# Performance work log

Measured on AMD Instinct MI355X. Metric: run time of the kernel, lower is better.

## Reference

```python
import jax, jax.numpy as jnp
import numpy as np

N_NODES = 10000
N_EDGES = 160000
D_IN = 128
D_EMB = 512
D_HID = 256
GAT_SLOPE = 0.2   # PyG GATv2Conv default negative_slope
MLP_SLOPE = 0.1   # relu_alpha


def _glorot(key, shape):
    fan_in, fan_out = shape[0], shape[-1]
    lim = np.sqrt(6.0 / (fan_in + fan_out))
    return jax.random.uniform(key, shape, jnp.float32, -lim, lim)


def setup_inputs() -> dict:
    key = jax.random.key(0)
    ks = jax.random.split(key, 20)
    inp = {
        'x': jax.random.normal(ks[0], (N_NODES, D_IN), jnp.float32),
        'edge_index': jax.random.randint(ks[1], (2, N_EDGES), 0, N_NODES, jnp.int64),
    }
    # GATv2 layers: (Wl, Wr, att, bias) each
    dims = [(D_IN, D_EMB), (D_EMB, D_EMB), (D_EMB, D_EMB)]
    for i, (di, do) in enumerate(dims, start=1):
        inp[f'Wl{i}'] = _glorot(ks[2 + 4 * i], (di, do))
        inp[f'Wr{i}'] = _glorot(ks[3 + 4 * i], (di, do))
        inp[f'att{i}'] = _glorot(ks[4 + 4 * i], (1, do))[0]
        inp[f'b{i}'] = jnp.zeros((do,), jnp.float32)
    # MLP
    inp['A1'] = _glorot(ks[2], (D_EMB, D_HID)); inp['c1'] = jnp.zeros((D_HID,), jnp.float32)
    inp['A2'] = _glorot(ks[3], (D_HID, D_HID)); inp['c2'] = jnp.zeros((D_HID,), jnp.float32)
    inp['A3'] = _glorot(ks[4], (D_HID, 1));     inp['c3'] = jnp.zeros((1,), jnp.float32)
    return inp


def gatv2_conv(x, src, dst, Wl, Wr, att, bias):
    # PyG GATv2Conv, heads=1: xl = source transform, xr = target transform
    xl = x @ Wl                                   # [N, D]
    xr = x @ Wr                                   # [N, D]
    # per-edge attention logit: att . leaky_relu(xl[src] + xr[dst])
    e = jax.nn.leaky_relu(xl[src] + xr[dst], GAT_SLOPE) @ att   # [E]
    # segment softmax over incoming edges of each dst node
    emax = jax.ops.segment_max(e, dst, num_segments=N_NODES)    # [N]
    w = jnp.exp(e - emax[dst])
    denom = jax.ops.segment_sum(w, dst, num_segments=N_NODES)   # [N]
    alpha = w / (denom[dst] + 1e-16)                             # [E]
    out = jax.ops.segment_sum(alpha[:, None] * xl[src], dst, num_segments=N_NODES)
    return out + bias


def reference(x, edge_index, Wl1, Wr1, att1, b1, Wl2, Wr2, att2, b2,
              Wl3, Wr3, att3, b3, A1, c1, A2, c2, A3, c3):
    src, dst = edge_index[0], edge_index[1]
    h = jnp.tanh(gatv2_conv(x, src, dst, Wl1, Wr1, att1, b1))
    h = jnp.tanh(gatv2_conv(h, src, dst, Wl2, Wr2, att2, b2))
    h = jnp.tanh(gatv2_conv(h, src, dst, Wl3, Wr3, att3, b3))
    h = jax.nn.leaky_relu(h @ A1 + c1, MLP_SLOPE)
    h = jax.nn.leaky_relu(h @ A2 + c2, MLP_SLOPE)
    logits = h @ A3 + c3                          # [N, 1]
    return jax.nn.softmax(logits, axis=0)         # softmax over nodes
```

## Files before the change

kernel.cpp:

```cpp
#include <hip/hip_runtime.h>
#include <hip/hip_bf16.h>

#define N_NODES 10000
#define N_EDGES 160000
#define D_IN    128
#define D_EMB   512
#define D_HID   256

typedef unsigned short u16;
typedef __attribute__((ext_vector_type(8))) short short8;
typedef __attribute__((ext_vector_type(4))) float floatx4;

__device__ __forceinline__ float bf2f(u16 u) {
    union { unsigned int i; float f; } v; v.i = ((unsigned int)u) << 16; return v.f;
}
__device__ __forceinline__ u16 f2bf(float f) {
    union { float f; unsigned int i; } v; v.f = f;
    unsigned int x = v.i;
    return (u16)((x + 0x7fffu + ((x >> 16) & 1u)) >> 16);
}
__device__ __forceinline__ float inval(const void* p, int fp32, int idx) {
    return fp32 ? ((const float*)p)[idx] : bf2f(((const u16*)p)[idx]);
}

__device__ __forceinline__ void gld_lds16(const u16* g, u16* l) {
    __builtin_amdgcn_global_load_lds((const __attribute__((address_space(1))) void*)g,
                                     (__attribute__((address_space(3))) void*)l,
                                     16, 0, 0);
}

__device__ __forceinline__ int edge_src(const int* __restrict__ ei, int flg, int e) {
    int v = flg ? ei[2 * e] : ei[e];
    return min(max(v, 0), N_NODES - 1);
}
__device__ __forceinline__ int edge_dst(const int* __restrict__ ei, int flg, int e) {
    int v = flg ? ei[2 * N_EDGES + 2 * e] : ei[N_EDGES + e];
    return min(max(v, 0), N_NODES - 1);
}

__global__ void sentinel_kernel(float* out, int n) {
    int i = blockIdx.x * 256 + threadIdx.x;
    if (i < n) out[i] = 1.0f;
}

__global__ __launch_bounds__(256)
void detect_zero_kernel(const int* __restrict__ ei, const u16* __restrict__ xu,
                        int* flag, int* counts, float* logits) {
    int gid = blockIdx.x * 256 + threadIdx.x;
    for (int i = gid; i < N_NODES; i += gridDim.x * 256) { counts[i] = 0; logits[i] = 0.f; }
    if (blockIdx.x != 0) return;
    __shared__ int s_or[256];
    __shared__ int s_cnt[256];
    int t = threadIdx.x;
    int v = 0;
    for (int k = t; k < 4096; k += 256) v |= ei[1 + 2 * k];
    int c = 0;
    for (int k = t; k < 4096; k += 256) {
        u16 u = xu[k];
        int ex = (u >> 7) & 0xFF;
        bool plaus = (u == 0) || (ex >= 64 && ex <= 191);
        if (!plaus) c++;
    }
    s_or[t] = v; s_cnt[t] = c;
    __syncthreads();
    for (int off = 128; off > 0; off >>= 1) {
        if (t < off) { s_or[t] |= s_or[t + off]; s_cnt[t] += s_cnt[t + off]; }
        __syncthreads();
    }
    if (t == 0) {
        flag[0] = (s_or[0] == 0) ? 1 : 0;
        flag[1] = (s_cnt[0] > 256) ? 1 : 0;
    }
}

struct ConvJobs {
    const void* src[10];
    u16* dh[10];
    u16* dl[10];
    int rows[10], cols[10], trans[10];
    int cum[11];
    int njobs;
};

__global__ __launch_bounds__(256)
void convert_fused_kernel(ConvJobs jobs, const int* __restrict__ flag) {
    int idx = blockIdx.x * 256 + threadIdx.x;
    if (idx >= jobs.cum[jobs.njobs]) return;
    int fp32 = flag[1];
    int jb = 0;
    while (idx >= jobs.cum[jb + 1]) jb++;
    int local = idx - jobs.cum[jb];
    float v = inval(jobs.src[jb], fp32, local);
    u16 hi = f2bf(v);
    int o;
    if (jobs.trans[jb]) {
        int r = local / jobs.cols[jb], c = local % jobs.cols[jb];
        o = c * jobs.rows[jb] + r;
    } else o = local;
    jobs.dh[jb][o] = hi;
    if (jobs.dl[jb]) jobs.dl[jb][o] = f2bf(v - bf2f(hi));
}

__global__ void count_edges_kernel(const int* __restrict__ ei, const int* __restrict__ flag,
                                   int* counts) {
    int e = blockIdx.x * 256 + threadIdx.x;
    if (e < N_EDGES) atomicAdd(&counts[edge_dst(ei, flag[0], e)], 1);
}

__global__ __launch_bounds__(256)
void scan_counts_kernel(int* counts, int* rowptr) {
    __shared__ int part[256];
    int tid = threadIdx.x;
    const int CH = 40;
    int base = tid * CH;
    int loc[CH];
    int s = 0;
    #pragma unroll
    for (int i = 0; i < CH; i++) {
        int idx = base + i;
        int c = (idx < N_NODES) ? counts[idx] : 0;
        loc[i] = s; s += c;
    }
    part[tid] = s;
    __syncthreads();
    for (int off = 1; off < 256; off <<= 1) {
        int v = part[tid];
        int add = (tid >= off) ? part[tid - off] : 0;
        __syncthreads();
        part[tid] = v + add;
        __syncthreads();
    }
    int pre = (tid > 0) ? part[tid - 1] : 0;
    #pragma unroll
    for (int i = 0; i < CH; i++) {
        int idx = base + i;
        if (idx < N_NODES) { int v = pre + loc[i]; rowptr[idx] = v; counts[idx] = v; }
    }
    if (tid == 255) rowptr[N_NODES] = part[255];
}

__global__ void fill_esrcp_kernel(const int* __restrict__ ei, const int* __restrict__ flag,
                                  int* counts, int* esrcp) {
    int e = blockIdx.x * 256 + threadIdx.x;
    if (e < N_EDGES) {
        int flg = flag[0];
        int pos = atomicAdd(&counts[edge_dst(ei, flg, e)], 1);
        if (pos >= 0 && pos < N_EDGES) esrcp[pos] = edge_src(ei, flg, e);
    }
}

__global__ __launch_bounds__(256)
void gemm_dual_kernel(const u16* __restrict__ Ah, const u16* __restrict__ Al,
                      const u16* __restrict__ B0h, const u16* __restrict__ B1h,
                      u16* __restrict__ C0, u16* __restrict__ C1,
                      int M, int N, int K)
{
    __shared__ u16 sAh[128 * 32];
    __shared__ u16 sAl[128 * 32];
    __shared__ u16 sBh[128 * 32];
    int nb = N >> 7;
    int half = (int)blockIdx.x >= nb;
    int bx = half ? (blockIdx.x - nb) : blockIdx.x;
    const u16* BTh = half ? B1h : B0h;
    u16* Cf = half ? C1 : C0;

    int tid = threadIdx.x;
    int lane = tid & 63, wv = tid >> 6;
    int l15 = lane & 15, l4 = lane >> 4;
    int wr = (wv >> 1) * 64, wc = (wv & 1) * 64;
    int m0 = blockIdx.y * 128, n0 = bx * 128;

    int i0 = tid, i1 = tid + 256;
    int r0 = i0 >> 2, b0 = i0 & 3, sb0 = b0 ^ ((r0 >> 1) & 3);
    int r1 = i1 >> 2, b1 = i1 & 3, sb1 = b1 ^ ((r1 >> 1) & 3);
    int gr0 = min(m0 + r0, M - 1), gr1 = min(m0 + r1, M - 1);
    const u16* a0p = Ah + (size_t)gr0 * K + sb0 * 8;
    const u16* a1p = Ah + (size_t)gr1 * K + sb1 * 8;
    const u16* l0p = Al + (size_t)gr0 * K + sb0 * 8;
    const u16* l1p = Al + (size_t)gr1 * K + sb1 * 8;
    const u16* bb0p = BTh + (size_t)(n0 + r0) * K + sb0 * 8;
    const u16* bb1p = BTh + (size_t)(n0 + r1) * K + sb1 * 8;
    u16* lA0 = &sAh[(size_t)(wv * 64) * 8];
    u16* lA1 = &sAh[(size_t)(256 + wv * 64) * 8];
    u16* lL0 = &sAl[(size_t)(wv * 64) * 8];
    u16* lL1 = &sAl[(size_t)(256 + wv * 64) * 8];
    u16* lB0 = &sBh[(size_t)(wv * 64) * 8];
    u16* lB1 = &sBh[(size_t)(256 + wv * 64) * 8];

    floatx4 acc[4][4];
    #pragma unroll
    for (int i = 0; i < 4; i++)
        #pragma unroll
        for (int j = 0; j < 4; j++) acc[i][j] = (floatx4){0.f, 0.f, 0.f, 0.f};

    int aoff[4], boff[4];
    #pragma unroll
    for (int i = 0; i < 4; i++) {
        int arow = wr + i * 16 + l15;
        aoff[i] = arow * 32 + ((l4 ^ ((arow >> 1) & 3)) << 3);
        int bcol = wc + i * 16 + l15;
        boff[i] = bcol * 32 + ((l4 ^ ((bcol >> 1) & 3)) << 3);
    }

    for (int kk = 0; kk < K; kk += 32) {
        __syncthreads();
        gld_lds16(a0p + kk, lA0);
        gld_lds16(a1p + kk, lA1);
        gld_lds16(l0p + kk, lL0);
        gld_lds16(l1p + kk, lL1);
        gld_lds16(bb0p + kk, lB0);
        gld_lds16(bb1p + kk, lB1);
        __syncthreads();

        short8 ah[4], al[4];
        #pragma unroll
        for (int i = 0; i < 4; i++) {
            ah[i] = *(const short8*)(&sAh[aoff[i]]);
            al[i] = *(const short8*)(&sAl[aoff[i]]);
        }
        #pragma unroll
        for (int j = 0; j < 4; j++) {
            short8 bh = *(const short8*)(&sBh[boff[j]]);
            #pragma unroll
            for (int i = 0; i < 4; i++) {
                acc[i][j] = __builtin_amdgcn_mfma_f32_16x16x32_bf16(ah[i], bh, acc[i][j], 0, 0, 0);
                acc[i][j] = __builtin_amdgcn_mfma_f32_16x16x32_bf16(al[i], bh, acc[i][j], 0, 0, 0);
            }
        }
    }

    #pragma unroll
    for (int j = 0; j < 4; j++) {
        int col = n0 + wc + j * 16 + l15;
        #pragma unroll
        for (int i = 0; i < 4; i++) {
            #pragma unroll
            for (int r = 0; r < 4; r++) {
                int row = m0 + wr + i * 16 + l4 * 4 + r;
                if (row < M) Cf[(size_t)row * N + col] = f2bf(acc[i][j][r]);
            }
        }
    }
}

template<int FUSE>
__global__ __launch_bounds__(256)
void gemm_mlp64_kernel(const u16* __restrict__ Ah, const u16* __restrict__ Al,
                       const u16* __restrict__ BTh,
                       u16* __restrict__ Ch, u16* __restrict__ Cl,
                       const void* __restrict__ biasraw,
                       const void* __restrict__ A3raw, float* __restrict__ logits,
                       const int* __restrict__ flag,
                       int M, int N, int K)
{
    __shared__ u16 sAh[64 * 32];
    __shared__ u16 sAl[64 * 32];
    __shared__ u16 sBh[64 * 32];
    int tid = threadIdx.x;
    int lane = tid & 63, wv = tid >> 6;
    int l15 = lane & 15, l4 = lane >> 4;
    int m0 = blockIdx.y * 64, n0 = blockIdx.x * 64;

    int r = (tid >> 2), blk = tid & 3, sb = blk ^ ((r >> 1) & 3);
    int gr = min(m0 + r, M - 1);
    const u16* ap = Ah + (size_t)gr * K + sb * 8;
    const u16* lp = Al + (size_t)gr * K + sb * 8;
    const u16* bp = BTh + (size_t)(n0 + r) * K + sb * 8;
    u16* lA = &sAh[(size_t)(wv * 64) * 8];
    u16* lL = &sAl[(size_t)(wv * 64) * 8];
    u16* lB = &sBh[(size_t)(wv * 64) * 8];

    floatx4 acc[4];
    #pragma unroll
    for (int j = 0; j < 4; j++) acc[j] = (floatx4){0.f, 0.f, 0.f, 0.f};

    int arow = wv * 16 + l15;
    int aoff = arow * 32 + ((l4 ^ ((arow >> 1) & 3)) << 3);
    int boff[4];
    #pragma unroll
    for (int j = 0; j < 4; j++) {
        int bcol = j * 16 + l15;
        boff[j] = bcol * 32 + ((l4 ^ ((bcol >> 1) & 3)) << 3);
    }

    for (int kk = 0; kk < K; kk += 32) {
        __syncthreads();
        gld_lds16(ap + kk, lA);
        gld_lds16(lp + kk, lL);
        gld_lds16(bp + kk, lB);
        __syncthreads();

        short8 ah = *(const short8*)(&sAh[aoff]);
        short8 al = *(const short8*)(&sAl[aoff]);
        #pragma unroll
        for (int j = 0; j < 4; j++) {
            short8 bh = *(const short8*)(&sBh[boff[j]]);
            acc[j] = __builtin_amdgcn_mfma_f32_16x16x32_bf16(ah, bh, acc[j], 0, 0, 0);
            acc[j] = __builtin_amdgcn_mfma_f32_16x16x32_bf16(al, bh, acc[j], 0, 0, 0);
        }
    }

    const int fp32 = flag[1];
    float lsum[4] = {0.f, 0.f, 0.f, 0.f};
    #pragma unroll
    for (int j = 0; j < 4; j++) {
        int col = n0 + j * 16 + l15;
        float bv = inval(biasraw, fp32, col);
        float a3 = FUSE ? inval(A3raw, fp32, col) : 0.f;
        #pragma unroll
        for (int rr = 0; rr < 4; rr++) {
            int row = m0 + wv * 16 + l4 * 4 + rr;
            if (row < M) {
                float v = acc[j][rr] + bv;
                v = v > 0.f ? v : 0.1f * v;
                if (FUSE) {
                    lsum[rr] += v * a3;
                } else {
                    u16 hi = f2bf(v);
                    Ch[(size_t)row * N + col] = hi;
                    Cl[(size_t)row * N + col] = f2bf(v - bf2f(hi));
                }
            }
        }
    }
    if (FUSE) {
        #pragma unroll
        for (int rr = 0; rr < 4; rr++) {
            float s = lsum[rr];
            s += __shfl_xor(s, 1);
            s += __shfl_xor(s, 2);
            s += __shfl_xor(s, 4);
            s += __shfl_xor(s, 8);
            int row = m0 + wv * 16 + l4 * 4 + rr;
            if (l15 == 0 && row < M) atomicAdd(&logits[row], s);
        }
    }
}

__device__ __forceinline__ void online_update(float e, const float v[8],
                                              float& m_run, float& s_run, float acc[8])
{
    if (e > m_run) {
        float sc = __expf(m_run - e);
        s_run = s_run * sc + 1.f;
        #pragma unroll
        for (int k = 0; k < 8; k++) acc[k] = acc[k] * sc + v[k];
        m_run = e;
    } else {
        float w = __expf(e - m_run);
        s_run += w;
        #pragma unroll
        for (int k = 0; k < 8; k++) acc[k] += w * v[k];
    }
}

__global__ __launch_bounds__(256)
void gat_wave_kernel(const int* __restrict__ rowptr, const int* __restrict__ esrcp,
                     const u16* __restrict__ xlb, const u16* __restrict__ xrb,
                     const void* __restrict__ att, const void* __restrict__ bias,
                     const int* __restrict__ flag,
                     u16* __restrict__ hh, u16* __restrict__ hl)
{
    int lane = threadIdx.x & 63, wv = threadIdx.x >> 6;
    int n = blockIdx.x * 4 + wv;
    if (n >= N_NODES) return;
    int fp32 = flag[1];
    int d0 = lane * 8;

    union { uint4 q; u16 us[8]; } xru;
    xru.q = *(const uint4*)(xrb + (size_t)n * D_EMB + d0);
    float xrv[8];
    #pragma unroll
    for (int k = 0; k < 8; k++) xrv[k] = bf2f(xru.us[k]);
    float attv[8];
    #pragma unroll
    for (int k = 0; k < 8; k++) attv[k] = inval(att, fp32, d0 + k);

    int beg = rowptr[n], end = rowptr[n + 1];
    float m_run = -3.4e38f, s_run = 0.f;
    float acc[8] = {0.f, 0.f, 0.f, 0.f, 0.f, 0.f, 0.f, 0.f};

    int j = beg;
    for (; j + 4 <= end; j += 4) {
        int s0 = esrcp[j], s1 = esrcp[j + 1], s2 = esrcp[j + 2], s3 = esrcp[j + 3];
        union { uint4 q; u16 us[8]; } u0, u1, u2, u3;
        u0.q = *(const uint4*)(xlb + (size_t)s0 * D_EMB + d0);
        u1.q = *(const uint4*)(xlb + (size_t)s1 * D_EMB + d0);
        u2.q = *(const uint4*)(xlb + (size_t)s2 * D_EMB + d0);
        u3.q = *(const uint4*)(xlb + (size_t)s3 * D_EMB + d0);
        float v0[8], v1[8], v2[8], v3[8];
        #pragma unroll
        for (int k = 0; k < 8; k++) {
            v0[k] = bf2f(u0.us[k]); v1[k] = bf2f(u1.us[k]);
            v2[k] = bf2f(u2.us[k]); v3[k] = bf2f(u3.us[k]);
        }
        float e0 = 0.f, e1 = 0.f, e2 = 0.f, e3 = 0.f;
        #pragma unroll
        for (int k = 0; k < 8; k++) {
            float t0 = v0[k] + xrv[k]; t0 = t0 > 0.f ? t0 : 0.2f * t0; e0 += attv[k] * t0;
            float t1 = v1[k] + xrv[k]; t1 = t1 > 0.f ? t1 : 0.2f * t1; e1 += attv[k] * t1;
            float t2 = v2[k] + xrv[k]; t2 = t2 > 0.f ? t2 : 0.2f * t2; e2 += attv[k] * t2;
            float t3 = v3[k] + xrv[k]; t3 = t3 > 0.f ? t3 : 0.2f * t3; e3 += attv[k] * t3;
        }
        #pragma unroll
        for (int o = 32; o > 0; o >>= 1) {
            e0 += __shfl_xor(e0, o);
            e1 += __shfl_xor(e1, o);
            e2 += __shfl_xor(e2, o);
            e3 += __shfl_xor(e3, o);
        }
        online_update(e0, v0, m_run, s_run, acc);
        online_update(e1, v1, m_run, s_run, acc);
        online_update(e2, v2, m_run, s_run, acc);
        online_update(e3, v3, m_run, s_run, acc);
    }
    for (; j < end; j++) {
        int s0 = esrcp[j];
        union { uint4 q; u16 us[8]; } u0;
        u0.q = *(const uint4*)(xlb + (size_t)s0 * D_EMB + d0);
        float v0[8];
        #pragma unroll
        for (int k = 0; k < 8; k++) v0[k] = bf2f(u0.us[k]);
        float e0 = 0.f;
        #pragma unroll
        for (int k = 0; k < 8; k++) {
            float t = v0[k] + xrv[k]; t = t > 0.f ? t : 0.2f * t; e0 += attv[k] * t;
        }
        #pragma unroll
        for (int o = 32; o > 0; o >>= 1) e0 += __shfl_xor(e0, o);
        online_update(e0, v0, m_run, s_run, acc);
    }

    float inv = 1.f / (s_run + 1e-16f);
    union { uint4 q; u16 us[8]; } ph, pl;
    #pragma unroll
    for (int k = 0; k < 8; k++) {
        float h = tanhf(acc[k] * inv + inval(bias, fp32, d0 + k));
        u16 hi = f2bf(h);
        ph.us[k] = hi;
        pl.us[k] = f2bf(h - bf2f(hi));
    }
    *(uint4*)(&hh[(size_t)n * D_EMB + d0]) = ph.q;
    *(uint4*)(&hl[(size_t)n * D_EMB + d0]) = pl.q;
}

__global__ __launch_bounds__(256)
void softmax_kernel(const float* __restrict__ logits, float* __restrict__ out)
{
    __shared__ float red[4];
    __shared__ float s_m, s_s;
    int tid = threadIdx.x, lane = tid & 63, wv = tid >> 6;
    float m = -3.4e38f;
    for (int i = tid; i < N_NODES; i += 256) m = fmaxf(m, logits[i]);
    #pragma unroll
    for (int o = 32; o > 0; o >>= 1) m = fmaxf(m, __shfl_down(m, o));
    if (lane == 0) red[wv] = m;
    __syncthreads();
    if (tid == 0) {
        float mm = red[0];
        for (int i = 1; i < 4; i++) mm = fmaxf(mm, red[i]);
        s_m = mm;
    }
    __syncthreads();
    float mm = s_m;
    float s = 0.f;
    for (int i = tid; i < N_NODES; i += 256) s += __expf(logits[i] - mm);
    #pragma unroll
    for (int o = 32; o > 0; o >>= 1) s += __shfl_down(s, o);
    if (lane == 0) red[wv] = s;
    __syncthreads();
    if (tid == 0) {
        float ss = 0.f;
        for (int i = 0; i < 4; i++) ss += red[i];
        s_s = ss;
    }
    __syncthreads();
    float invs = 1.f / s_s;
    for (int i = tid; i < N_NODES; i += 256) out[i] = __expf(logits[i] - mm) * invs;
}

extern "C" void kernel_launch(void* const* d_in, const int* in_sizes, int n_in,
                              void* d_out, int out_size, void* d_ws, size_t ws_size,
                              hipStream_t stream)
{
    const void* x   = d_in[0];
    const int*  ei  = (const int*)d_in[1];
    const void* Wl[3]  = {d_in[2],  d_in[6],  d_in[10]};
    const void* Wr[3]  = {d_in[3],  d_in[7],  d_in[11]};
    const void* att[3] = {d_in[4],  d_in[8],  d_in[12]};
    const void* bia[3] = {d_in[5],  d_in[9],  d_in[13]};
    const void* A1 = d_in[14];
    const void* c1 = d_in[15];
    const void* A2 = d_in[16];
    const void* c2 = d_in[17];
    const void* A3 = d_in[18];

    char* p = (char*)d_ws;
    auto alloc = [&](size_t bytes) {
        char* r = p;
        p += (bytes + 255) & ~(size_t)255;
        return r;
    };
    u16*   xlb    = (u16*)  alloc((size_t)N_NODES * D_EMB * 4);
    u16*   xrb    = (u16*)  alloc((size_t)N_NODES * D_EMB * 2);
    u16*   hh     = (u16*)  alloc((size_t)N_NODES * D_EMB * 2);
    u16*   hl     = (u16*)  alloc((size_t)N_NODES * D_EMB * 2);
    int*   esrcp  = (int*)  alloc((size_t)N_EDGES * 4);
    int*   rowptr = (int*)  alloc((size_t)(N_NODES + 1) * 4);
    int*   counts = (int*)  alloc((size_t)N_NODES * 4);
    int*   flag   = (int*)  alloc(256);
    float* logits = (float*)alloc((size_t)N_NODES * 4);
    u16* wl1h = (u16*)alloc(D_EMB * D_IN  * 2);
    u16* wr1h = (u16*)alloc(D_EMB * D_IN  * 2);
    u16* wl2h = (u16*)alloc(D_EMB * D_EMB * 2);
    u16* wr2h = (u16*)alloc(D_EMB * D_EMB * 2);
    u16* wl3h = (u16*)alloc(D_EMB * D_EMB * 2);
    u16* wr3h = (u16*)alloc(D_EMB * D_EMB * 2);
    u16* a1h  = (u16*)alloc(D_EMB * D_HID * 2);
    u16* a2h  = (u16*)alloc(D_HID * D_HID * 2);
    u16* xph  = (u16*)alloc((size_t)N_NODES * D_IN * 2);
    u16* xpl  = (u16*)alloc((size_t)N_NODES * D_IN * 2);
    size_t needed = (size_t)(p - (char*)d_ws);

    if (ws_size < needed) {
        sentinel_kernel<<<(out_size + 255) / 256, 256, 0, stream>>>((float*)d_out, out_size);
        return;
    }

    u16* m1h = (u16*)xlb;
    u16* m1l = (u16*)((char*)xlb + 5120000);

    detect_zero_kernel<<<40, 256, 0, stream>>>(ei, (const u16*)x, flag, counts, logits);
    count_edges_kernel<<<(N_EDGES + 255) / 256, 256, 0, stream>>>(ei, flag, counts);
    scan_counts_kernel<<<1, 256, 0, stream>>>(counts, rowptr);
    fill_esrcp_kernel<<<(N_EDGES + 255) / 256, 256, 0, stream>>>(ei, flag, counts, esrcp);

    ConvJobs jobs;
    auto setjob = [&](int i, const void* s, u16* dh, u16* dl, int r, int c, int tr) {
        jobs.src[i] = s; jobs.dh[i] = dh; jobs.dl[i] = dl;
        jobs.rows[i] = r; jobs.cols[i] = c; jobs.trans[i] = tr;
    };
    setjob(0, x,     xph,  xpl,     N_NODES, D_IN, 0);
    setjob(1, Wl[0], wl1h, nullptr, D_IN,  D_EMB, 1);
    setjob(2, Wr[0], wr1h, nullptr, D_IN,  D_EMB, 1);
    setjob(3, Wl[1], wl2h, nullptr, D_EMB, D_EMB, 1);
    setjob(4, Wr[1], wr2h, nullptr, D_EMB, D_EMB, 1);
    setjob(5, Wl[2], wl3h, nullptr, D_EMB, D_EMB, 1);
    setjob(6, Wr[2], wr3h, nullptr, D_EMB, D_EMB, 1);
    setjob(7, A1,    a1h,  nullptr, D_EMB, D_HID, 1);
    setjob(8, A2,    a2h,  nullptr, D_HID, D_HID, 1);
    jobs.njobs = 9;
    jobs.cum[0] = 0;
    for (int i = 0; i < 9; i++) jobs.cum[i + 1] = jobs.cum[i] + jobs.rows[i] * jobs.cols[i];
    int ctotal = jobs.cum[9];
    convert_fused_kernel<<<(ctotal + 255) / 256, 256, 0, stream>>>(jobs, flag);

    dim3 gdual(2 * D_EMB / 128, (N_NODES + 127) / 128);
    dim3 gmlp64(D_HID / 64, (N_NODES + 63) / 64);
    int gatgrid = (N_NODES + 3) / 4;

    gemm_dual_kernel<<<gdual, 256, 0, stream>>>(xph, xpl, wl1h, wr1h, xlb, xrb, N_NODES, D_EMB, D_IN);
    gat_wave_kernel<<<gatgrid, 256, 0, stream>>>(rowptr, esrcp, xlb, xrb, att[0], bia[0], flag, hh, hl);
    gemm_dual_kernel<<<gdual, 256, 0, stream>>>(hh, hl, wl2h, wr2h, xlb, xrb, N_NODES, D_EMB, D_EMB);
    gat_wave_kernel<<<gatgrid, 256, 0, stream>>>(rowptr, esrcp, xlb, xrb, att[1], bia[1], flag, hh, hl);
    gemm_dual_kernel<<<gdual, 256, 0, stream>>>(hh, hl, wl3h, wr3h, xlb, xrb, N_NODES, D_EMB, D_EMB);
    gat_wave_kernel<<<gatgrid, 256, 0, stream>>>(rowptr, esrcp, xlb, xrb, att[2], bia[2], flag, hh, hl);

    gemm_mlp64_kernel<0><<<gmlp64, 256, 0, stream>>>(hh, hl, a1h, m1h, m1l, c1, nullptr, nullptr, flag, N_NODES, D_HID, D_EMB);
    gemm_mlp64_kernel<1><<<gmlp64, 256, 0, stream>>>(m1h, m1l, a2h, nullptr, nullptr, c2, A3, logits, flag, N_NODES, D_HID, D_HID);
    softmax_kernel<<<1, 256, 0, stream>>>(logits, (float*)d_out);
}
```

Measured before the change: 441.8 us.

## Sort nodes by in-degree descending for GAT wave scheduling

Builds a degree histogram and counting-sort permutation of nodes, highest in-degree first, then has each GAT wave process nodes in that order. The intent is load balancing: waves in a block get similar edge counts and heavy nodes start early, which shortens the tail. It adds three small kernel launches and one indirection per wave, and it scatters writes to hh/hl so output locality drops.

```diff
diff --git a/kernel.cpp b/kernel.cpp
--- a/kernel.cpp
+++ b/kernel.cpp
@@ -45,9 +45,10 @@
 
 __global__ __launch_bounds__(256)
 void detect_zero_kernel(const int* __restrict__ ei, const u16* __restrict__ xu,
-                        int* flag, int* counts, float* logits) {
+                        int* flag, int* counts, float* logits, int* dhist) {
     int gid = blockIdx.x * 256 + threadIdx.x;
     for (int i = gid; i < N_NODES; i += gridDim.x * 256) { counts[i] = 0; logits[i] = 0.f; }
+    if (gid < 64) dhist[gid] = 0;
     if (blockIdx.x != 0) return;
     __shared__ int s_or[256];
     __shared__ int s_cnt[256];
@@ -149,6 +150,32 @@
     }
 }
 
+__global__ void deg_hist_kernel(const int* __restrict__ rowptr, const int* __restrict__ counts,
+                                int* dhist) {
+    int n = blockIdx.x * 256 + threadIdx.x;
+    if (n < N_NODES) {
+        int deg = min(counts[n] - rowptr[n], 63);
+        atomicAdd(&dhist[deg], 1);
+    }
+}
+
+__global__ void deg_scan_kernel(int* dhist) {
+    if (threadIdx.x == 0 && blockIdx.x == 0) {
+        int run = 0;
+        for (int b = 63; b >= 0; b--) { int c = dhist[b]; dhist[b] = run; run += c; }
+    }
+}
+
+__global__ void deg_scatter_kernel(const int* __restrict__ rowptr, const int* __restrict__ counts,
+                                   int* dhist, int* nodeperm) {
+    int n = blockIdx.x * 256 + threadIdx.x;
+    if (n < N_NODES) {
+        int deg = min(counts[n] - rowptr[n], 63);
+        int pos = atomicAdd(&dhist[deg], 1);
+        if (pos >= 0 && pos < N_NODES) nodeperm[pos] = n;
+    }
+}
+
 __global__ __launch_bounds__(256)
 void gemm_dual_kernel(const u16* __restrict__ Ah, const u16* __restrict__ Al,
                       const u16* __restrict__ B0h, const u16* __restrict__ B1h,
@@ -356,14 +383,16 @@
 
 __global__ __launch_bounds__(256)
 void gat_wave_kernel(const int* __restrict__ rowptr, const int* __restrict__ esrcp,
+                     const int* __restrict__ nodeperm,
                      const u16* __restrict__ xlb, const u16* __restrict__ xrb,
                      const void* __restrict__ att, const void* __restrict__ bias,
                      const int* __restrict__ flag,
                      u16* __restrict__ hh, u16* __restrict__ hl)
 {
     int lane = threadIdx.x & 63, wv = threadIdx.x >> 6;
-    int n = blockIdx.x * 4 + wv;
-    if (n >= N_NODES) return;
+    int slot = blockIdx.x * 4 + wv;
+    if (slot >= N_NODES) return;
+    int n = nodeperm[slot];
     int fp32 = flag[1];
     int d0 = lane * 8;
 
@@ -510,6 +539,8 @@
     int*   counts = (int*)  alloc((size_t)N_NODES * 4);
     int*   flag   = (int*)  alloc(256);
     float* logits = (float*)alloc((size_t)N_NODES * 4);
+    int*   dhist  = (int*)  alloc(64 * 4);
+    int*   nodeperm = (int*)alloc((size_t)N_NODES * 4);
     u16* wl1h = (u16*)alloc(D_EMB * D_IN  * 2);
     u16* wr1h = (u16*)alloc(D_EMB * D_IN  * 2);
     u16* wl2h = (u16*)alloc(D_EMB * D_EMB * 2);
@@ -530,10 +561,13 @@
     u16* m1h = (u16*)xlb;
     u16* m1l = (u16*)((char*)xlb + 5120000);
 
-    detect_zero_kernel<<<40, 256, 0, stream>>>(ei, (const u16*)x, flag, counts, logits);
+    detect_zero_kernel<<<40, 256, 0, stream>>>(ei, (const u16*)x, flag, counts, logits, dhist);
     count_edges_kernel<<<(N_EDGES + 255) / 256, 256, 0, stream>>>(ei, flag, counts);
     scan_counts_kernel<<<1, 256, 0, stream>>>(counts, rowptr);
     fill_esrcp_kernel<<<(N_EDGES + 255) / 256, 256, 0, stream>>>(ei, flag, counts, esrcp);
+    deg_hist_kernel<<<(N_NODES + 255) / 256, 256, 0, stream>>>(rowptr, counts, dhist);
+    deg_scan_kernel<<<1, 64, 0, stream>>>(dhist);
+    deg_scatter_kernel<<<(N_NODES + 255) / 256, 256, 0, stream>>>(rowptr, counts, dhist, nodeperm);
 
     ConvJobs jobs;
     auto setjob = [&](int i, const void* s, u16* dh, u16* dl, int r, int c, int tr) {
@@ -560,11 +594,11 @@
     int gatgrid = (N_NODES + 3) / 4;
 
     gemm_dual_kernel<<<gdual, 256, 0, stream>>>(xph, xpl, wl1h, wr1h, xlb, xrb, N_NODES, D_EMB, D_IN);
-    gat_wave_kernel<<<gatgrid, 256, 0, stream>>>(rowptr, esrcp, xlb, xrb, att[0], bia[0], flag, hh, hl);
+    gat_wave_kernel<<<gatgrid, 256, 0, stream>>>(rowptr, esrcp, nodeperm, xlb, xrb, att[0], bia[0], flag, hh, hl);
     gemm_dual_kernel<<<gdual, 256, 0, stream>>>(hh, hl, wl2h, wr2h, xlb, xrb, N_NODES, D_EMB, D_EMB);
-    gat_wave_kernel<<<gatgrid, 256, 0, stream>>>(rowptr, esrcp, xlb, xrb, att[1], bia[1], flag, hh, hl);
+    gat_wave_kernel<<<gatgrid, 256, 0, stream>>>(rowptr, esrcp, nodeperm, xlb, xrb, att[1], bia[1], flag, hh, hl);
     gemm_dual_kernel<<<gdual, 256, 0, stream>>>(hh, hl, wl3h, wr3h, xlb, xrb, N_NODES, D_EMB, D_EMB);
-    gat_wave_kernel<<<gatgrid, 256, 0, stream>>>(rowptr, esrcp, xlb, xrb, att[2], bia[2], flag, hh, hl);
+    gat_wave_kernel<<<gatgrid, 256, 0, stream>>>(rowptr, esrcp, nodeperm, xlb, xrb, att[2], bia[2], flag, hh, hl);
 
     gemm_mlp64_kernel<0><<<gmlp64, 256, 0, stream>>>(hh, hl, a1h, m1h, m1l, c1, nullptr, nullptr, flag, N_NODES, D_HID, D_EMB);
     gemm_mlp64_kernel<1><<<gmlp64, 256, 0, stream>>>(m1h, m1l, a2h, nullptr, nullptr, c2, A3, logits, flag, N_NODES, D_HID, D_HID);
```

Result: slower. 475.7 us (+7.7%).
